# Performance work log

Hardware: AMD Instinct MI355X
Metric: run time of the kernel (lower is better)

Reference implementation:

```python
import jax, jax.numpy as jnp
import numpy as np

LN_EPS = 1e-5

def setup_inputs() -> dict:
    key = jax.random.key(0)
    B, T, D, H, NB = 32, 384, 512, 16, 5  # NB = 5 MHSA blocks actually used
    ks = jax.random.split(key, 10)
    s = 1.0 / np.sqrt(D)
    def w(k, shape):
        return jax.random.normal(k, shape, jnp.float32) * s
    return {
        "x": jax.random.normal(ks[0], (B, T, D), jnp.float32),
        # stacked params for the 5 used MHSA blocks, order:
        # [tmp_attn, layer1_1, layer1_2, layer1_3, layer2_1]
        "qw": w(ks[1], (NB, D, D)), "qb": w(ks[2], (NB, D)),
        "kw": w(ks[3], (NB, D, D)), "kb": w(ks[4], (NB, D)),
        "vw": w(ks[5], (NB, D, D)), "vb": w(ks[6], (NB, D)),
        "temp": jnp.ones((NB, H, 1, 1), jnp.float32),
        "ln_g": jnp.ones((D,), jnp.float32),
        "ln_b": jnp.zeros((D,), jnp.float32),
        "fus_w": w(ks[7], (D, D)), "fus_b": w(ks[8], (D,)),
        "num_heads": H,
    }


def _mhsa(x, wq, bq, wk, bk, wv, bv, temp, H):
    # Faithful to torch: .view(B, H, D//H, T) is a flat reshape of (B,T,D).
    B, T, D = x.shape
    d = D // H
    q = (x @ wq.T + bq).reshape(B, H, d, T)
    k = (x @ wk.T + bk).reshape(B, H, d, T)
    v = (x @ wv.T + bv).reshape(B, H, d, T)
    # k^T @ v -> (B,H,T,T), scaled by per-head temperature, softmax over last dim
    attn = jax.nn.softmax(jnp.einsum("bhdt,bhds->bhts", k, v) * temp, axis=-1)
    out = jnp.einsum("bhdt,bhts->bhds", q, attn)  # (B,H,d,T)
    return out.reshape(B, T, D)


def _layernorm(x, g, b):
    mu = jnp.mean(x, axis=-1, keepdims=True)
    var = jnp.mean(jnp.square(x - mu), axis=-1, keepdims=True)
    return (x - mu) * jax.lax.rsqrt(var + LN_EPS) * g + b


def reference(x, qw, qb, kw, kb, vw, vb, temp, ln_g, ln_b, fus_w, fus_b, num_heads):
    H = num_heads
    blk = lambda i, z: _mhsa(z, qw[i], qb[i], kw[i], kb[i], vw[i], vb[i], temp[i], H)
    x_ = blk(0, x)
    c1, c2, c3 = jnp.split(x, 3, axis=1)
    tmp_layer1 = jnp.concatenate([blk(1, c1), blk(2, c2), blk(3, c3)], axis=1) + x_
    tmp_layer2 = blk(4, _layernorm(tmp_layer1, ln_g, ln_b)) + x_
    alpha = jnp.stack([tmp_layer1, tmp_layer2], axis=0)  # (2,B,T,D)
    alpha = alpha @ fus_w.T + fus_b
    alpha = jax.nn.softmax(alpha, axis=0)
    return tmp_layer1 * alpha[0] + tmp_layer2 * alpha[1]
```

## Files before the change

kernel.cpp:

```cpp
#include <hip/hip_runtime.h>

typedef __attribute__((ext_vector_type(8))) _Float16 half8;
typedef __attribute__((ext_vector_type(4))) _Float16 half4v;
typedef __attribute__((ext_vector_type(2))) _Float16 half2v;
typedef __attribute__((ext_vector_type(4))) float float4v;

__device__ __forceinline__ float4v mfma16x16x32_f16(half8 a, half8 b, float4v c) {
#if defined(__HIP_DEVICE_COMPILE__)
#if __has_builtin(__builtin_amdgcn_mfma_f32_16x16x32_f16)
  return __builtin_amdgcn_mfma_f32_16x16x32_f16(a, b, c, 0, 0, 0);
#elif __has_builtin(__builtin_amdgcn_mfma_f32_16x16x32f16)
  return __builtin_amdgcn_mfma_f32_16x16x32f16(a, b, c, 0, 0, 0);
#else
#error "no 16x16x32 f16 mfma"
#endif
#else
  (void)a; (void)b;
  return c;
#endif
}

__device__ __forceinline__ float4v mfma16x16x16_f16(half4v a, half4v b, float4v c) {
#if defined(__HIP_DEVICE_COMPILE__)
#if __has_builtin(__builtin_amdgcn_mfma_f32_16x16x16f16)
  return __builtin_amdgcn_mfma_f32_16x16x16f16(a, b, c, 0, 0, 0);
#elif __has_builtin(__builtin_amdgcn_mfma_f32_16x16x16_f16)
  return __builtin_amdgcn_mfma_f32_16x16x16_f16(a, b, c, 0, 0, 0);
#else
#error "no 16x16x16 f16 mfma"
#endif
#else
  (void)a; (void)b;
  return c;
#endif
}

__device__ __forceinline__ void gl_lds16(const unsigned short* g, unsigned short* l) {
#if defined(__HIP_DEVICE_COMPILE__)
#if __has_builtin(__builtin_amdgcn_global_load_lds)
  __builtin_amdgcn_global_load_lds(
      (const __attribute__((address_space(1))) unsigned int*)g,
      (__attribute__((address_space(3))) unsigned int*)l, 16, 0, 0);
#else
  *(uint4*)l = *(const uint4*)g;
#endif
#else
  (void)g; (void)l;
#endif
}

__device__ __forceinline__ float fexp2(float x) {
#if defined(__HIP_DEVICE_COMPILE__)
#if __has_builtin(__builtin_amdgcn_exp2f)
  return __builtin_amdgcn_exp2f(x);
#else
  return __expf(x * 0.6931471805599453f);
#endif
#else
  return x;
#endif
}

__device__ __forceinline__ float frcp(float x) {
#if defined(__HIP_DEVICE_COMPILE__)
#if __has_builtin(__builtin_amdgcn_rcpf)
  return __builtin_amdgcn_rcpf(x);
#else
  return 1.0f / x;
#endif
#else
  return 1.0f / x;
#endif
}

__device__ __forceinline__ half2v pk_f16(float a, float b) {
#if defined(__HIP_DEVICE_COMPILE__)
#if __has_builtin(__builtin_amdgcn_cvt_pkrtz)
  return __builtin_bit_cast(half2v, __builtin_amdgcn_cvt_pkrtz(a, b));
#else
  half2v r;
  r[0] = (_Float16)a;
  r[1] = (_Float16)b;
  return r;
#endif
#else
  half2v r;
  r[0] = (_Float16)a;
  r[1] = (_Float16)b;
  return r;
#endif
}

__device__ __forceinline__ unsigned short f2h(float f) {
  union { _Float16 h; unsigned short u; } v;
  v.h = (_Float16)f;
  return v.u;
}

__device__ __forceinline__ float row_sum16(float x) {
#if defined(__HIP_DEVICE_COMPILE__)
#if __has_builtin(__builtin_amdgcn_update_dpp)
  int v;
  v = __builtin_bit_cast(int, x);
  x += __builtin_bit_cast(float, __builtin_amdgcn_update_dpp(0, v, 0x128, 0xF, 0xF, true));
  v = __builtin_bit_cast(int, x);
  x += __builtin_bit_cast(float, __builtin_amdgcn_update_dpp(0, v, 0x124, 0xF, 0xF, true));
  v = __builtin_bit_cast(int, x);
  x += __builtin_bit_cast(float, __builtin_amdgcn_update_dpp(0, v, 0x122, 0xF, 0xF, true));
  v = __builtin_bit_cast(int, x);
  x += __builtin_bit_cast(float, __builtin_amdgcn_update_dpp(0, v, 0x121, 0xF, 0xF, true));
  return x;
#else
  x += __shfl_xor(x, 1);
  x += __shfl_xor(x, 2);
  x += __shfl_xor(x, 4);
  x += __shfl_xor(x, 8);
  return x;
#endif
#else
  return x;
#endif
}

__global__ __launch_bounds__(256) void cvt_multi(
    const float* __restrict__ s0, unsigned short* __restrict__ d0, int n0,
    const float* __restrict__ s1, unsigned short* __restrict__ d1,
    const float* __restrict__ s2, unsigned short* __restrict__ d2,
    const float* __restrict__ s3, unsigned short* __restrict__ d3, int n13,
    const float* __restrict__ s4, unsigned short* __restrict__ d4, int n4c) {
  const int y = blockIdx.y;
  const float* s;
  unsigned short* d;
  int n;
  if (y == 0) { s = s0; d = d0; n = n0; }
  else if (y == 1) { s = s1; d = d1; n = n13; }
  else if (y == 2) { s = s2; d = d2; n = n13; }
  else if (y == 3) { s = s3; d = d3; n = n13; }
  else { s = s4; d = d4; n = n4c; }
  const int i = blockIdx.x * 256 + threadIdx.x;
  if (i >= n) return;
  float4 v = ((const float4*)s)[i];
  uint2 o;
  o.x = (unsigned)f2h(v.x) | ((unsigned)f2h(v.y) << 16);
  o.y = (unsigned)f2h(v.z) | ((unsigned)f2h(v.w) << 16);
  ((uint2*)d)[i] = o;
}

#define GEMM_CORE(WGPTR)                                                               \
  for (int k0 = 0; k0 < 512; k0 += 64) {                                               \
    _Pragma("unroll") for (int rnd = 0; rnd < 4; ++rnd) {                              \
      const int slot = rnd * 512 + tid;                                                \
      const int r = slot >> 3;                                                         \
      const int c = (slot & 7) ^ (r & 7);                                              \
      const size_t src = ((r >> 7) ? xrow1 : xrow0) + (size_t)(r & 127) * 512 +        \
                         (size_t)(k0 + c * 8);                                         \
      gl_lds16(Xbase + src, &Xs[slot * 8]);                                            \
    }                                                                                  \
    _Pragma("unroll") for (int rnd = 0; rnd < 2; ++rnd) {                              \
      const int s2 = rnd * 512 + tid;                                                  \
      const int r = s2 >> 3;                                                           \
      const int c = (s2 & 7) ^ (r & 7);                                                \
      gl_lds16((WGPTR) + (size_t)r * 512 + k0 + c * 8, &Wt[s2 * 8]);                   \
    }                                                                                  \
    __syncthreads();                                                                   \
    _Pragma("unroll") for (int kk = 0; kk < 2; ++kk) {                                 \
      half8 af[4], bf[4];                                                              \
      const int ch = ((kk * 4 + grp) ^ (col & 7)) * 8;                                 \
      _Pragma("unroll") for (int i = 0; i < 4; ++i)                                    \
          af[i] = *(const half8*)&Xs[(wm + i * 16 + col) * 64 + ch];                   \
      _Pragma("unroll") for (int j = 0; j < 4; ++j)                                    \
          bf[j] = *(const half8*)&Wt[(wn + j * 16 + col) * 64 + ch];                   \
      _Pragma("unroll") for (int i = 0; i < 4; ++i)                                    \
          _Pragma("unroll") for (int j = 0; j < 4; ++j)                                \
              acc[i][j] = mfma16x16x32_f16(af[i], bf[j], acc[i][j]);                   \
    }                                                                                  \
    __syncthreads();                                                                   \
  }

__global__ __launch_bounds__(512) void gemm_qkv6(
    const unsigned short* __restrict__ X,
    const unsigned short* __restrict__ Wq, const unsigned short* __restrict__ Wk,
    const unsigned short* __restrict__ Wv,
    const float* __restrict__ bq, const float* __restrict__ bk, const float* __restrict__ bv,
    unsigned short* __restrict__ CqA, unsigned short* __restrict__ CkA,
    unsigned short* __restrict__ CvA, unsigned short* __restrict__ CqB,
    unsigned short* __restrict__ CkB, unsigned short* __restrict__ CvB,
    int widx_fixed) {
  const int nt = blockIdx.x, mt = blockIdx.y, z = blockIdx.z;
  const int zz = z % 3, mode = z / 3;
  const unsigned short* W = (zz == 0) ? Wq : ((zz == 1) ? Wk : Wv);
  const float* bias = (zz == 0) ? bq : ((zz == 1) ? bk : bv);
  unsigned short* C = mode ? ((zz == 0) ? CqB : ((zz == 1) ? CkB : CvB))
                           : ((zz == 0) ? CqA : ((zz == 1) ? CkA : CvA));
  const int cpart = mt % 3, bb = (mt / 3) * 2;
  const int widx = mode ? (1 + cpart) : widx_fixed;
  W += (size_t)widx * 512 * 512;
  bias += widx * 512;

  const size_t grow0 = (size_t)bb * 384 + cpart * 128;
  const size_t grow1 = grow0 + 384;
  const size_t xrow0 = grow0 * 512, xrow1 = grow1 * 512;
  const unsigned short* Xbase = X;

  __shared__ __align__(16) unsigned short Xs[2048 * 8];
  __shared__ __align__(16) unsigned short Wt[1024 * 8];
  const int tid = threadIdx.x, lane = tid & 63, w = tid >> 6;
  const int col = lane & 15, grp = lane >> 4;
  const int wm = (w >> 1) * 64, wn = (w & 1) * 64;

  const float4v zero4 = {0.f, 0.f, 0.f, 0.f};
  float4v acc[4][4];
#pragma unroll
  for (int i = 0; i < 4; ++i)
#pragma unroll
    for (int j = 0; j < 4; ++j) acc[i][j] = zero4;

  GEMM_CORE(W + (size_t)nt * 128 * 512)

#pragma unroll
  for (int j = 0; j < 4; ++j) {
    const int n = nt * 128 + wn + j * 16 + col;
    const float bj = bias[n];
#pragma unroll
    for (int i = 0; i < 4; ++i)
#pragma unroll
      for (int r = 0; r < 4; ++r) {
        const int m = wm + i * 16 + grp * 4 + r;
        const size_t grow = ((m >> 7) ? grow1 : grow0) + (m & 127);
        C[grow * 512 + n] = f2h(acc[i][j][r] + bj);
      }
  }
}

__global__ __launch_bounds__(512) void gemm_fusion(
    const unsigned short* __restrict__ X, const unsigned short* __restrict__ Wf,
    const float* __restrict__ dif, const float* __restrict__ tl2, float* __restrict__ outp) {
  const int nt = blockIdx.x, mt = blockIdx.y;
  const size_t grow0 = (size_t)mt * 256, grow1 = grow0 + 128;
  const size_t xrow0 = grow0 * 512, xrow1 = grow1 * 512;
  const unsigned short* Xbase = X;

  __shared__ __align__(16) unsigned short Xs[2048 * 8];
  __shared__ __align__(16) unsigned short Wt[1024 * 8];
  const int tid = threadIdx.x, lane = tid & 63, w = tid >> 6;
  const int col = lane & 15, grp = lane >> 4;
  const int wm = (w >> 1) * 64, wn = (w & 1) * 64;

  const float4v zero4 = {0.f, 0.f, 0.f, 0.f};
  float4v acc[4][4];
#pragma unroll
  for (int i = 0; i < 4; ++i)
#pragma unroll
    for (int j = 0; j < 4; ++j) acc[i][j] = zero4;

  GEMM_CORE(Wf + (size_t)nt * 128 * 512)

#pragma unroll
  for (int j = 0; j < 4; ++j) {
    const int n = nt * 128 + wn + j * 16 + col;
#pragma unroll
    for (int i = 0; i < 4; ++i)
#pragma unroll
      for (int r = 0; r < 4; ++r) {
        const int m = wm + i * 16 + grp * 4 + r;
        const size_t off = (((m >> 7) ? grow1 : grow0) + (m & 127)) * 512 + n;
        const float d = dif[off], t2 = tl2[off];
        const float sg = 1.0f / (1.0f + __expf(-acc[i][j][r]));
        outp[off] = t2 + d * sg;
      }
  }
}

template <int T>
__device__ __forceinline__ void attn_body(
    const unsigned short* __restrict__ Qb, const unsigned short* __restrict__ Kb,
    const unsigned short* __restrict__ Vb, const float* __restrict__ temp_base,
    const float* add_src,
    float* outp, int chunk_elems, int cb, int h, int b,
    const float* tl1_src,
    unsigned short* diff16, float* diff32,
    unsigned short* KVt, float* Zs) {
  constexpr int NT = T / 16;
  constexpr int NSW = NT / 8;
  constexpr int SLAB = T * 32;
  const int base = b * (384 * 512) + cb * chunk_elems + h * SLAB;
  const float tl2e = temp_base[cb * 16 + h] * 1.4426950408889634f;

  const int tid = threadIdx.x, lane = tid & 63, w = tid >> 6;
  const int col = lane & 15, grp = lane >> 4;

  if (tid < NT * 16) Zs[tid] = 0.f;

  {
    const unsigned short* src = Kb + base;
    constexpr int ITER = (T * 4) / 512;
#pragma unroll
    for (int p = 0; p < ITER; ++p) {
      const int f = p * 512 + tid;
      const int t = f >> 2, blk = (f & 3) * 8;
      unsigned short tmp[8];
#pragma unroll
      for (int i = 0; i < 8; ++i) tmp[i] = src[(size_t)(blk + i) * T + t];
      *(uint4*)&KVt[t * 40 + blk] = *(const uint4*)tmp;
    }
  }
  half8 vfr[NSW];
  {
    const unsigned short* Vg = Vb + base;
#pragma unroll
    for (int si = 0; si < NSW; ++si) {
      const int s = (w + si * 8) * 16 + col;
      union { unsigned short u[8]; half8 v; } t8;
#pragma unroll
      for (int i = 0; i < 8; ++i) t8.u[i] = Vg[(size_t)(grp * 8 + i) * T + s];
      vfr[si] = t8.v;
    }
  }
  __syncthreads();

  const float4v zero4 = {0.f, 0.f, 0.f, 0.f};

#pragma unroll 2
  for (int tt = 0; tt < NT; ++tt) {
    half8 kf = *(const half8*)&KVt[(tt * 16 + col) * 40 + grp * 8];
    float z0 = 0.f, z1 = 0.f, z2 = 0.f, z3 = 0.f;
#pragma unroll
    for (int si = 0; si < NSW; ++si) {
      float4v sv = mfma16x16x32_f16(kf, vfr[si], zero4);
      z0 += fexp2(sv[0] * tl2e);
      z1 += fexp2(sv[1] * tl2e);
      z2 += fexp2(sv[2] * tl2e);
      z3 += fexp2(sv[3] * tl2e);
    }
    z0 = row_sum16(z0);
    z1 = row_sum16(z1);
    z2 = row_sum16(z2);
    z3 = row_sum16(z3);
    if (col == 0) {
      float* zp = &Zs[tt * 16 + grp * 4];
      atomicAdd(zp + 0, z0);
      atomicAdd(zp + 1, z1);
      atomicAdd(zp + 2, z2);
      atomicAdd(zp + 3, z3);
    }
  }
  __syncthreads();

  const unsigned short* Qsl = Qb + base;
  float4v oacc[NSW][2];
#pragma unroll
  for (int si = 0; si < NSW; ++si) {
    oacc[si][0] = zero4;
    oacc[si][1] = zero4;
  }
#pragma unroll 2
  for (int tt = 0; tt < NT; ++tt) {
    const int toff = tt * 16 + grp * 4;
    half4v qa0 = *(const half4v*)(Qsl + col * T + toff);
    half4v qa1 = *(const half4v*)(Qsl + (16 + col) * T + toff);
    float4v zsv = *(const float4v*)&Zs[tt * 16 + grp * 4];
    const float zi0 = frcp(zsv[0]), zi1 = frcp(zsv[1]), zi2 = frcp(zsv[2]),
                zi3 = frcp(zsv[3]);
    half8 kf = *(const half8*)&KVt[(tt * 16 + col) * 40 + grp * 8];
#pragma unroll
    for (int si = 0; si < NSW; ++si) {
      float4v sv = mfma16x16x32_f16(kf, vfr[si], zero4);
      half2v lo = pk_f16(fexp2(sv[0] * tl2e) * zi0, fexp2(sv[1] * tl2e) * zi1);
      half2v hi = pk_f16(fexp2(sv[2] * tl2e) * zi2, fexp2(sv[3] * tl2e) * zi3);
      half4v pb = __builtin_shufflevector(lo, hi, 0, 1, 2, 3);
      oacc[si][0] = mfma16x16x16_f16(qa0, pb, oacc[si][0]);
      oacc[si][1] = mfma16x16x16_f16(qa1, pb, oacc[si][1]);
    }
  }

#pragma unroll
  for (int si = 0; si < NSW; ++si) {
    const int s = (w + si * 8) * 16 + col;
#pragma unroll
    for (int m0 = 0; m0 < 2; ++m0) {
#pragma unroll
      for (int r = 0; r < 4; ++r) {
        const int dd = m0 * 16 + grp * 4 + r;
        const int off = base + dd * T + s;
        const float o = oacc[si][m0][r];
        float v = o;
        if (add_src) v += add_src[off];
        if (tl1_src) {
          const float d = tl1_src[off] - o;
          diff16[off] = f2h(d);
          diff32[off] = d;
        }
        outp[off] = v;
      }
    }
  }
}

__global__ __launch_bounds__(512) void attn_merged(
    const unsigned short* __restrict__ Q0, const unsigned short* __restrict__ K0,
    const unsigned short* __restrict__ V0, const unsigned short* __restrict__ Qc,
    const unsigned short* __restrict__ Kc, const unsigned short* __restrict__ Vc,
    const float* __restrict__ temp, float* xres, float* tl1) {
  __shared__ __align__(16) unsigned short Ks[384 * 40];
  __shared__ __align__(16) float Zs[24 * 16];
  const int id = blockIdx.x + 16 * (blockIdx.y + 32 * blockIdx.z);
  const int part = id & 3, rest = id >> 2;
  const int h = rest & 15, b = rest >> 4;
  if (part == 0)
    attn_body<384>(Q0, K0, V0, temp, nullptr, xres, 0, 0, h, b,
                   nullptr, nullptr, nullptr, Ks, Zs);
  else
    attn_body<128>(Qc, Kc, Vc, temp + 16, nullptr, tl1, 128 * 512, part - 1, h, b,
                   nullptr, nullptr, nullptr, Ks, Zs);
}

__global__ __launch_bounds__(512) void attn_tail(
    const unsigned short* __restrict__ Q, const unsigned short* __restrict__ K,
    const unsigned short* __restrict__ V, const float* __restrict__ temp4,
    const float* add_src, float* tl12, unsigned short* __restrict__ diff16,
    float* diff32) {
  __shared__ __align__(16) unsigned short Ks[384 * 40];
  __shared__ __align__(16) float Zs[24 * 16];
  attn_body<384>(Q, K, V, temp4, add_src, tl12, 0, 0, blockIdx.x, blockIdx.y,
                 tl12, diff16, diff32, Ks, Zs);
}

__global__ __launch_bounds__(256) void ln_kernel(const float* __restrict__ a,
                                                 const float* __restrict__ c,
                                                 const float* __restrict__ g,
                                                 const float* __restrict__ bb,
                                                 unsigned short* __restrict__ y) {
  const int row = blockIdx.x * 4 + (threadIdx.x >> 6);
  const int lane = threadIdx.x & 63;
  const float* ar = a + (size_t)row * 512;
  const float* cr = c + (size_t)row * 512;
  float4 a0 = *(const float4*)&ar[lane * 8];
  float4 a1 = *(const float4*)&ar[lane * 8 + 4];
  float4 c0 = *(const float4*)&cr[lane * 8];
  float4 c1 = *(const float4*)&cr[lane * 8 + 4];
  float4 v0, v1;
  v0.x = a0.x + c0.x; v0.y = a0.y + c0.y; v0.z = a0.z + c0.z; v0.w = a0.w + c0.w;
  v1.x = a1.x + c1.x; v1.y = a1.y + c1.y; v1.z = a1.z + c1.z; v1.w = a1.w + c1.w;
  float s = v0.x + v0.y + v0.z + v0.w + v1.x + v1.y + v1.z + v1.w;
  float q = v0.x * v0.x + v0.y * v0.y + v0.z * v0.z + v0.w * v0.w +
            v1.x * v1.x + v1.y * v1.y + v1.z * v1.z + v1.w * v1.w;
#pragma unroll
  for (int m = 1; m < 64; m <<= 1) {
    s += __shfl_xor(s, m);
    q += __shfl_xor(q, m);
  }
  const float mean = s * (1.0f / 512.0f);
  const float var = q * (1.0f / 512.0f) - mean * mean;
  const float rs = rsqrtf(var + 1e-5f);
  float4 g0 = *(const float4*)&g[lane * 8];
  float4 g1 = *(const float4*)&g[lane * 8 + 4];
  float4 b0 = *(const float4*)&bb[lane * 8];
  float4 b1 = *(const float4*)&bb[lane * 8 + 4];
  uint4 o;
  o.x = (unsigned)f2h((v0.x - mean) * rs * g0.x + b0.x) |
        ((unsigned)f2h((v0.y - mean) * rs * g0.y + b0.y) << 16);
  o.y = (unsigned)f2h((v0.z - mean) * rs * g0.z + b0.z) |
        ((unsigned)f2h((v0.w - mean) * rs * g0.w + b0.w) << 16);
  o.z = (unsigned)f2h((v1.x - mean) * rs * g1.x + b1.x) |
        ((unsigned)f2h((v1.y - mean) * rs * g1.y + b1.y) << 16);
  o.w = (unsigned)f2h((v1.z - mean) * rs * g1.z + b1.z) |
        ((unsigned)f2h((v1.w - mean) * rs * g1.w + b1.w) << 16);
  *(uint4*)&y[(size_t)row * 512 + lane * 8] = o;
}

extern "C" void kernel_launch(void* const* d_in, const int* in_sizes, int n_in,
                              void* d_out, int out_size, void* d_ws, size_t ws_size,
                              hipStream_t stream) {
  const float* x = (const float*)d_in[0];
  const float* qw = (const float*)d_in[1];
  const float* qb = (const float*)d_in[2];
  const float* kw = (const float*)d_in[3];
  const float* kb = (const float*)d_in[4];
  const float* vw = (const float*)d_in[5];
  const float* vb = (const float*)d_in[6];
  const float* temp = (const float*)d_in[7];
  const float* ln_g = (const float*)d_in[8];
  const float* ln_b = (const float*)d_in[9];
  const float* fus_w = (const float*)d_in[10];
  float* out = (float*)d_out;

  const size_t NE = (size_t)32 * 384 * 512;
  const size_t WE = (size_t)5 * 512 * 512;

  char* p = (char*)d_ws;
  auto alloc = [&](size_t bytes) {
    char* r = p;
    p += (bytes + 255) & ~(size_t)255;
    return r;
  };
  unsigned short* xb = (unsigned short*)alloc(NE * 2);
  unsigned short* wqb = (unsigned short*)alloc(WE * 2);
  unsigned short* wkb = (unsigned short*)alloc(WE * 2);
  unsigned short* wvb = (unsigned short*)alloc(WE * 2);
  unsigned short* fwb = (unsigned short*)alloc((size_t)512 * 512 * 2);
  unsigned short* Qb = (unsigned short*)alloc(NE * 2);
  unsigned short* Kb = (unsigned short*)alloc(NE * 2);
  unsigned short* Vb = (unsigned short*)alloc(NE * 2);
  float* xres = (float*)alloc(NE * 4);
  float* tl1 = (float*)alloc(NE * 4);
  unsigned short* yb = (unsigned short*)alloc(NE * 2);

  unsigned short* Qc = yb;
  unsigned short* Kc = (unsigned short*)out;
  unsigned short* Vc = Kc + NE;

  cvt_multi<<<dim3((int)(NE / 4 / 256), 5), 256, 0, stream>>>(
      x, xb, (int)(NE / 4), qw, wqb, kw, wkb, vw, wvb, (int)(WE / 4), fus_w, fwb,
      512 * 512 / 4);

  gemm_qkv6<<<dim3(4, 48, 6), 512, 0, stream>>>(xb, wqb, wkb, wvb, qb, kb, vb,
                                                Qb, Kb, Vb, Qc, Kc, Vc, 0);
  attn_merged<<<dim3(16, 32, 4), 512, 0, stream>>>(Qb, Kb, Vb, Qc, Kc, Vc, temp,
                                                   xres, tl1);
  ln_kernel<<<12288 / 4, 256, 0, stream>>>(tl1, xres, ln_g, ln_b, yb);
  gemm_qkv6<<<dim3(4, 48, 3), 512, 0, stream>>>(yb, wqb, wkb, wvb, qb, kb, vb,
                                                Qb, Kb, Vb, Qb, Kb, Vb, 4);
  attn_tail<<<dim3(16, 32, 1), 512, 0, stream>>>(Qb, Kb, Vb, temp + 64, xres, tl1,
                                                 yb, xres);
  gemm_fusion<<<dim3(4, 48), 512, 0, stream>>>(yb, fwb, xres, tl1, out);

  (void)in_sizes; (void)n_in; (void)out_size; (void)ws_size;
}
```

Measured before the change: 410.6 us.

## Fuse softmax passes: compute scores once, keep probabilities in registers

Replaces the two-pass attention (a full pass computing exp sums, then recomputing scores and exps) with a grouped single pass. Each group of NB row tiles computes the scores once, subtracts a per-wave row max, stores unnormalised fp16 probabilities in registers, and accumulates the rescaled partial sums atomically. After a barrier it folds the normalisation (exp(max)/Z) into the Q operand before the PV MFMA. This removes the duplicated QK MFMA and exp work. In exchange it adds a barrier per group, register pressure from holding the probability tiles, and fp16 rounding of the max and scale factors.

```diff
diff --git a/kernel.cpp b/kernel.cpp
--- a/kernel.cpp
+++ b/kernel.cpp
@@ -115,6 +115,31 @@
   x += __shfl_xor(x, 2);
   x += __shfl_xor(x, 4);
   x += __shfl_xor(x, 8);
+  return x;
+#endif
+#else
+  return x;
+#endif
+}
+
+__device__ __forceinline__ float row_max16(float x) {
+#if defined(__HIP_DEVICE_COMPILE__)
+#if __has_builtin(__builtin_amdgcn_update_dpp)
+  int v;
+  v = __builtin_bit_cast(int, x);
+  x = fmaxf(x, __builtin_bit_cast(float, __builtin_amdgcn_update_dpp(0, v, 0x128, 0xF, 0xF, true)));
+  v = __builtin_bit_cast(int, x);
+  x = fmaxf(x, __builtin_bit_cast(float, __builtin_amdgcn_update_dpp(0, v, 0x124, 0xF, 0xF, true)));
+  v = __builtin_bit_cast(int, x);
+  x = fmaxf(x, __builtin_bit_cast(float, __builtin_amdgcn_update_dpp(0, v, 0x122, 0xF, 0xF, true)));
+  v = __builtin_bit_cast(int, x);
+  x = fmaxf(x, __builtin_bit_cast(float, __builtin_amdgcn_update_dpp(0, v, 0x121, 0xF, 0xF, true)));
+  return x;
+#else
+  x = fmaxf(x, __shfl_xor(x, 1));
+  x = fmaxf(x, __shfl_xor(x, 2));
+  x = fmaxf(x, __shfl_xor(x, 4));
+  x = fmaxf(x, __shfl_xor(x, 8));
   return x;
 #endif
 #else
@@ -271,7 +296,7 @@
   }
 }
 
-template <int T>
+template <int T, int NB>
 __device__ __forceinline__ void attn_body(
     const unsigned short* __restrict__ Qb, const unsigned short* __restrict__ Kb,
     const unsigned short* __restrict__ Vb, const float* __restrict__ temp_base,
@@ -319,33 +344,6 @@
   __syncthreads();
 
   const float4v zero4 = {0.f, 0.f, 0.f, 0.f};
-
-#pragma unroll 2
-  for (int tt = 0; tt < NT; ++tt) {
-    half8 kf = *(const half8*)&KVt[(tt * 16 + col) * 40 + grp * 8];
-    float z0 = 0.f, z1 = 0.f, z2 = 0.f, z3 = 0.f;
-#pragma unroll
-    for (int si = 0; si < NSW; ++si) {
-      float4v sv = mfma16x16x32_f16(kf, vfr[si], zero4);
-      z0 += fexp2(sv[0] * tl2e);
-      z1 += fexp2(sv[1] * tl2e);
-      z2 += fexp2(sv[2] * tl2e);
-      z3 += fexp2(sv[3] * tl2e);
-    }
-    z0 = row_sum16(z0);
-    z1 = row_sum16(z1);
-    z2 = row_sum16(z2);
-    z3 = row_sum16(z3);
-    if (col == 0) {
-      float* zp = &Zs[tt * 16 + grp * 4];
-      atomicAdd(zp + 0, z0);
-      atomicAdd(zp + 1, z1);
-      atomicAdd(zp + 2, z2);
-      atomicAdd(zp + 3, z3);
-    }
-  }
-  __syncthreads();
-
   const unsigned short* Qsl = Qb + base;
   float4v oacc[NSW][2];
 #pragma unroll
@@ -353,23 +351,79 @@
     oacc[si][0] = zero4;
     oacc[si][1] = zero4;
   }
-#pragma unroll 2
-  for (int tt = 0; tt < NT; ++tt) {
-    const int toff = tt * 16 + grp * 4;
-    half4v qa0 = *(const half4v*)(Qsl + col * T + toff);
-    half4v qa1 = *(const half4v*)(Qsl + (16 + col) * T + toff);
-    float4v zsv = *(const float4v*)&Zs[tt * 16 + grp * 4];
-    const float zi0 = frcp(zsv[0]), zi1 = frcp(zsv[1]), zi2 = frcp(zsv[2]),
-                zi3 = frcp(zsv[3]);
-    half8 kf = *(const half8*)&KVt[(tt * 16 + col) * 40 + grp * 8];
-#pragma unroll
-    for (int si = 0; si < NSW; ++si) {
-      float4v sv = mfma16x16x32_f16(kf, vfr[si], zero4);
-      half2v lo = pk_f16(fexp2(sv[0] * tl2e) * zi0, fexp2(sv[1] * tl2e) * zi1);
-      half2v hi = pk_f16(fexp2(sv[2] * tl2e) * zi2, fexp2(sv[3] * tl2e) * zi3);
-      half4v pb = __builtin_shufflevector(lo, hi, 0, 1, 2, 3);
-      oacc[si][0] = mfma16x16x16_f16(qa0, pb, oacc[si][0]);
-      oacc[si][1] = mfma16x16x16_f16(qa1, pb, oacc[si][1]);
+
+  for (int g = 0; g < NT / NB; ++g) {
+    half4v ph[NB][NSW];
+    half4v mh[NB];
+#pragma unroll
+    for (int u = 0; u < NB; ++u) {
+      const int tt = g * NB + u;
+      half8 kf = *(const half8*)&KVt[(tt * 16 + col) * 40 + grp * 8];
+      float4v sv[NSW];
+#pragma unroll
+      for (int si = 0; si < NSW; ++si) sv[si] = mfma16x16x32_f16(kf, vfr[si], zero4);
+      float4v mx = sv[0];
+#pragma unroll
+      for (int si = 1; si < NSW; ++si) {
+        mx[0] = fmaxf(mx[0], sv[si][0]);
+        mx[1] = fmaxf(mx[1], sv[si][1]);
+        mx[2] = fmaxf(mx[2], sv[si][2]);
+        mx[3] = fmaxf(mx[3], sv[si][3]);
+      }
+      const float m0 = row_max16(mx[0]) * tl2e;
+      const float m1 = row_max16(mx[1]) * tl2e;
+      const float m2 = row_max16(mx[2]) * tl2e;
+      const float m3 = row_max16(mx[3]) * tl2e;
+      const half4v mhu = __builtin_shufflevector(pk_f16(m0, m1), pk_f16(m2, m3), 0, 1, 2, 3);
+      mh[u] = mhu;
+      const float mf0 = (float)mhu[0], mf1 = (float)mhu[1], mf2 = (float)mhu[2],
+                  mf3 = (float)mhu[3];
+      float z0 = 0.f, z1 = 0.f, z2 = 0.f, z3 = 0.f;
+#pragma unroll
+      for (int si = 0; si < NSW; ++si) {
+        const float e0 = fexp2(sv[si][0] * tl2e - mf0);
+        const float e1 = fexp2(sv[si][1] * tl2e - mf1);
+        const float e2 = fexp2(sv[si][2] * tl2e - mf2);
+        const float e3 = fexp2(sv[si][3] * tl2e - mf3);
+        z0 += e0;
+        z1 += e1;
+        z2 += e2;
+        z3 += e3;
+        ph[u][si] = __builtin_shufflevector(pk_f16(e0, e1), pk_f16(e2, e3), 0, 1, 2, 3);
+      }
+      z0 = row_sum16(z0);
+      z1 = row_sum16(z1);
+      z2 = row_sum16(z2);
+      z3 = row_sum16(z3);
+      if (col == 0) {
+        float* zp = &Zs[tt * 16 + grp * 4];
+        atomicAdd(zp + 0, z0 * fexp2(mf0));
+        atomicAdd(zp + 1, z1 * fexp2(mf1));
+        atomicAdd(zp + 2, z2 * fexp2(mf2));
+        atomicAdd(zp + 3, z3 * fexp2(mf3));
+      }
+    }
+    __syncthreads();
+#pragma unroll
+    for (int u = 0; u < NB; ++u) {
+      const int tt = g * NB + u;
+      const int toff = tt * 16 + grp * 4;
+      half4v qa0 = *(const half4v*)(Qsl + col * T + toff);
+      half4v qa1 = *(const half4v*)(Qsl + (16 + col) * T + toff);
+      float4v zsv = *(const float4v*)&Zs[tt * 16 + grp * 4];
+      const half4v mhu = mh[u];
+      const float c0 = fexp2((float)mhu[0]) * frcp(zsv[0]);
+      const float c1 = fexp2((float)mhu[1]) * frcp(zsv[1]);
+      const float c2 = fexp2((float)mhu[2]) * frcp(zsv[2]);
+      const float c3 = fexp2((float)mhu[3]) * frcp(zsv[3]);
+      const half4v c4 = __builtin_shufflevector(pk_f16(c0, c1), pk_f16(c2, c3), 0, 1, 2, 3);
+      qa0 = qa0 * c4;
+      qa1 = qa1 * c4;
+#pragma unroll
+      for (int si = 0; si < NSW; ++si) {
+        oacc[si][0] = mfma16x16x16_f16(qa0, ph[u][si], oacc[si][0]);
+        oacc[si][1] = mfma16x16x16_f16(qa1, ph[u][si], oacc[si][1]);
+      }
     }
   }
 
@@ -407,11 +461,11 @@
   const int part = id & 3, rest = id >> 2;
   const int h = rest & 15, b = rest >> 4;
   if (part == 0)
-    attn_body<384>(Q0, K0, V0, temp, nullptr, xres, 0, 0, h, b,
-                   nullptr, nullptr, nullptr, Ks, Zs);
+    attn_body<384, 2>(Q0, K0, V0, temp, nullptr, xres, 0, 0, h, b,
+                      nullptr, nullptr, nullptr, Ks, Zs);
   else
-    attn_body<128>(Qc, Kc, Vc, temp + 16, nullptr, tl1, 128 * 512, part - 1, h, b,
-                   nullptr, nullptr, nullptr, Ks, Zs);
+    attn_body<128, 2>(Qc, Kc, Vc, temp + 16, nullptr, tl1, 128 * 512, part - 1, h, b,
+                      nullptr, nullptr, nullptr, Ks, Zs);
 }
 
 __global__ __launch_bounds__(512) void attn_tail(
@@ -421,8 +475,8 @@
     float* diff32) {
   __shared__ __align__(16) unsigned short Ks[384 * 40];
   __shared__ __align__(16) float Zs[24 * 16];
-  attn_body<384>(Q, K, V, temp4, add_src, tl12, 0, 0, blockIdx.x, blockIdx.y,
-                 tl12, diff16, diff32, Ks, Zs);
+  attn_body<384, 2>(Q, K, V, temp4, add_src, tl12, 0, 0, blockIdx.x, blockIdx.y,
+                    tl12, diff16, diff32, Ks, Zs);
 }
 
 __global__ __launch_bounds__(256) void ln_kernel(const float* __restrict__ a,
```

Measured after the change: 472.3 us. +15.0%, slower.
